# Kernel optimization log

Measured on AMD Instinct MI355X. Metric: run time of the kernel, lower is better.

## Reference

```python
import jax, jax.numpy as jnp
import numpy as np

B, T, D, H = 1024, 128, 300, 100
FORGET_BIAS = 1.0


def _lstm_final_c(x, W, b):
    """Run a BasicLSTMCell over x:[B,T,D]; return final cell state c:[B,H].
    Gate order (TF BasicLSTMCell): i, j, f, o from [x,h] @ W + b, W:[D+H,4H].
    """
    Bv = x.shape[0]
    c0 = jnp.zeros((Bv, H), x.dtype)
    h0 = jnp.zeros((Bv, H), x.dtype)

    def step(carry, xt):
        c, h = carry
        z = jnp.concatenate([xt, h], axis=-1) @ W + b  # [B,4H]
        i, j, f, o = jnp.split(z, 4, axis=-1)
        c2 = c * jax.nn.sigmoid(f + FORGET_BIAS) + jax.nn.sigmoid(i) * jnp.tanh(j)
        h2 = jnp.tanh(c2) * jax.nn.sigmoid(o)
        return (c2, h2), None

    (cT, _), _ = jax.lax.scan(step, (c0, h0), jnp.swapaxes(x, 0, 1))  # scan over time
    return cT


def _bi_rnn_c(x, W_fw, b_fw, W_bw, b_bw):
    # full sequence_length => backward cell consumes time-reversed input
    c_fw = _lstm_final_c(x, W_fw, b_fw)
    c_bw = _lstm_final_c(x[:, ::-1, :], W_bw, b_bw)
    return jnp.concatenate([c_fw, c_bw], axis=1)  # [B,2H]


def setup_inputs() -> dict:
    key = jax.random.key(0)
    ks = jax.random.split(key, 6)
    s = 0.05
    return {
        "premises": jax.random.normal(ks[0], (B, T, D), jnp.float32),
        "hypotheses": jax.random.normal(ks[1], (B, T, D), jnp.float32),
        "Wp_fw": jax.random.normal(ks[2], (D + H, 4 * H), jnp.float32) * s,
        "bp_fw": jnp.zeros((4 * H,), jnp.float32),
        "Wp_bw": jax.random.normal(ks[3], (D + H, 4 * H), jnp.float32) * s,
        "bp_bw": jnp.zeros((4 * H,), jnp.float32),
        "Wh_fw": jax.random.normal(ks[4], (D + H, 4 * H), jnp.float32) * s,
        "bh_fw": jnp.zeros((4 * H,), jnp.float32),
        "Wh_bw": jax.random.normal(ks[5], (D + H, 4 * H), jnp.float32) * s,
        "bh_bw": jnp.zeros((4 * H,), jnp.float32),
    }


def reference(premises, hypotheses, Wp_fw, bp_fw, Wp_bw, bp_bw,
              Wh_fw, bh_fw, Wh_bw, bh_bw):
    premise_out = _bi_rnn_c(premises, Wp_fw, bp_fw, Wp_bw, bp_bw)      # [B,2H]
    hypothesis_out = _bi_rnn_c(hypotheses, Wh_fw, bh_fw, Wh_bw, bh_bw)  # [B,2H]
    return jnp.concatenate([premise_out, hypothesis_out], axis=1)      # [B,4H]
```

## Files before the change

kernel.cpp:

```cpp
#include <hip/hip_runtime.h>
#include <hip/hip_bf16.h>

#define T_STEPS 128
#define D_IN    300
#define H_DIM   100
#define KDIM    400
#define KSTRIDE 424
#define NTILES  25
#define WAVES   12
#define BLOCK   (WAVES * 64)
#define MROWS   16
#define LN2E    1.44269504f
#define LN2E2   2.88539008f

typedef __attribute__((ext_vector_type(8))) short bf16x8;
typedef __attribute__((ext_vector_type(4))) float f32x4;

__device__ __forceinline__ ushort f2bf(float f) {
    uint u = __float_as_uint(f);
    u += 0x7FFFu + ((u >> 16) & 1u);
    return (ushort)(u >> 16);
}
__device__ __forceinline__ uint cvt_pk_bf16(float lo, float hi) {
    uint r;
    asm("v_cvt_pk_bf16_f32 %0, %1, %2" : "=v"(r) : "v"(lo), "v"(hi));
    return r;
}

__device__ __forceinline__ float lstm_gate(const f32x4 z, float& c) {
    float ei = __builtin_amdgcn_exp2f(-z[0]);
    float ej = __builtin_amdgcn_exp2f(fminf(-z[1], 126.0f));
    float ef = __builtin_amdgcn_exp2f(-z[2]);
    float eo = __builtin_amdgcn_exp2f(-z[3]);
    float rf  = __builtin_amdgcn_rcpf(1.0f + ef);
    float rij = __builtin_amdgcn_rcpf((1.0f + ei) * (1.0f + ej));
    float c2 = c * rf + (1.0f - ej) * rij;
    c = c2;
    float ec = __builtin_amdgcn_exp2f(fminf(-LN2E2 * c2, 126.0f));
    return (1.0f - ec) * __builtin_amdgcn_rcpf((1.0f + ec) * (1.0f + eo));
}

__global__ __launch_bounds__(256) void prep_w(
    const float* __restrict__ W0, const float* __restrict__ W1,
    const float* __restrict__ W2, const float* __restrict__ W3,
    ushort* __restrict__ Wt)
{
    int idx = blockIdx.x * 256 + threadIdx.x;
    const int total = 4 * 400 * KSTRIDE;
    if (idx >= total) return;
    int c   = idx / (400 * KSTRIDE);
    int rem = idx - c * (400 * KSTRIDE);
    int p   = rem / KSTRIDE;
    int k   = rem - p * KSTRIDE;
    const float* W = (c == 0) ? W0 : (c == 1) ? W1 : (c == 2) ? W2 : W3;
    const int g = p & 3;
    const float scale = (g == 1) ? LN2E2 : LN2E;
    float v = 0.0f;
    if (k < KDIM) v = W[k * 400 + g * 100 + (p >> 2)] * scale;
    Wt[idx] = f2bf(v);
}

__global__ __launch_bounds__(BLOCK) void lstm_mfma(
    const float* __restrict__ premises,
    const float* __restrict__ hypotheses,
    const float* __restrict__ b0, const float* __restrict__ b1,
    const float* __restrict__ b2, const float* __restrict__ b3,
    const ushort* __restrict__ Wt,
    float* __restrict__ out)
{
    __shared__ ushort xh[2][MROWS * KSTRIDE];
    __shared__ ushort b24[13 * 512];

    const int tid = threadIdx.x;
    const int l   = tid & 63;
    const int w   = tid >> 6;
    const int combo = blockIdx.y;
    const int row0  = blockIdx.x * MROWS;
    const bool backward = (combo & 1) != 0;
    const float* x    = (combo < 2) ? premises : hypotheses;
    const float* bias = (combo == 0) ? b0 : (combo == 1) ? b1 : (combo == 2) ? b2 : b3;
    const ushort* Wc  = Wt + (size_t)combo * 400 * KSTRIDE;

    const int bn = l & 15;
    const int ul = l >> 4;

    const int nt0 = 2 * w, nt1 = 2 * w + 1;
    bf16x8 bfr0[13], bfr1[13];
    {
        const ushort* bp = Wc + (size_t)(nt0 * 16 + bn) * KSTRIDE + ul * 8;
        #pragma unroll
        for (int ks = 0; ks < 13; ++ks)
            bfr0[ks] = *reinterpret_cast<const bf16x8*>(bp + ks * 32);
    }
    {
        const ushort* bp = Wc + (size_t)(nt1 * 16 + bn) * KSTRIDE + ul * 8;
        #pragma unroll
        for (int ks = 0; ks < 13; ++ks)
            bfr1[ks] = *reinterpret_cast<const bf16x8*>(bp + ks * 32);
    }
    const bool hasS = (w == WAVES - 1);

    if (w == 0) {
        const ushort* bp = Wc + (size_t)(24 * 16 + bn) * KSTRIDE + ul * 8;
        #pragma unroll
        for (int ks = 0; ks < 13; ++ks)
            *reinterpret_cast<bf16x8*>(&b24[ks * 512 + l * 8]) =
                *reinterpret_cast<const bf16x8*>(bp + ks * 32);
    }

    float bva[4], bvb[4], bvS[4] = {0.f, 0.f, 0.f, 0.f};
    {
        int u = nt0 * 4 + ul;
        bva[0] = LN2E * bias[u];
        bva[1] = LN2E2 * bias[100 + u];
        bva[2] = LN2E * (bias[200 + u] + 1.0f);
        bva[3] = LN2E * bias[300 + u];
        u = nt1 * 4 + ul;
        bvb[0] = LN2E * bias[u];
        bvb[1] = LN2E2 * bias[100 + u];
        bvb[2] = LN2E * (bias[200 + u] + 1.0f);
        bvb[3] = LN2E * bias[300 + u];
        if (hasS) {
            u = 96 + ul;
            bvS[0] = LN2E * bias[u];
            bvS[1] = LN2E2 * bias[100 + u];
            bvS[2] = LN2E * (bias[200 + u] + 1.0f);
            bvS[3] = LN2E * bias[300 + u];
        }
    }

    for (int i = tid; i < 2 * MROWS * (KSTRIDE - KDIM); i += BLOCK) {
        int b = i / (MROWS * (KSTRIDE - KDIM));
        int j = i - b * (MROWS * (KSTRIDE - KDIM));
        int r = j / (KSTRIDE - KDIM);
        int k = KDIM + (j - r * (KSTRIDE - KDIM));
        xh[b][r * KSTRIDE + k] = 0;
    }
    for (int i = tid; i < MROWS * H_DIM; i += BLOCK) {
        int r = i / H_DIM;
        xh[0][r * KSTRIDE + D_IN + (i - r * H_DIM)] = 0;
    }
    {
        int t0 = backward ? (T_STEPS - 1) : 0;
        for (int c = tid; c < 1200; c += BLOCK) {
            int r = c / 75, cc = c - (c / 75) * 75;
            float4 v = *reinterpret_cast<const float4*>(
                x + ((size_t)(row0 + r) * T_STEPS + t0) * D_IN + cc * 4);
            uint2 q;
            q.x = cvt_pk_bf16(v.x, v.y);
            q.y = cvt_pk_bf16(v.z, v.w);
            *reinterpret_cast<uint2*>(&xh[0][r * KSTRIDE + cc * 4]) = q;
        }
    }
    __syncthreads();

    const uint a_off = (uint)(l & 15) * KSTRIDE + (uint)(l >> 4) * 8;
    const int  row   = l & 15;
    const int sc0 = tid, sc1 = tid + BLOCK;
    const int sr0 = sc0 / 75, sd0 = sc0 - sr0 * 75;
    const int sr1 = sc1 / 75, sd1 = sc1 - sr1 * 75;
    const bool has1 = (sc1 < 1200);

    float creg0 = 0.f, creg1 = 0.f, cregS = 0.f;

    for (int t = 0; t < T_STEPS; ++t) {
        const ushort* cur = &xh[t & 1][0];
        ushort* nxt = &xh[(t & 1) ^ 1][0];

        float4 p0, p1;
        if (t < T_STEPS - 1) {
            int tn = backward ? (T_STEPS - 2 - t) : (t + 1);
            p0 = *reinterpret_cast<const float4*>(
                x + ((size_t)(row0 + sr0) * T_STEPS + tn) * D_IN + sd0 * 4);
            if (has1)
                p1 = *reinterpret_cast<const float4*>(
                    x + ((size_t)(row0 + sr1) * T_STEPS + tn) * D_IN + sd1 * 4);
        }

        f32x4 acc0 = {bva[0], bva[1], bva[2], bva[3]};
        f32x4 acc1 = {bvb[0], bvb[1], bvb[2], bvb[3]};
        f32x4 accS = {bvS[0], bvS[1], bvS[2], bvS[3]};
        #pragma unroll
        for (int ks = 0; ks < 13; ++ks) {
            const bf16x8 a = *reinterpret_cast<const bf16x8*>(cur + a_off + ks * 32);
            acc0 = __builtin_amdgcn_mfma_f32_16x16x32_bf16(bfr0[ks], a, acc0, 0, 0, 0);
            acc1 = __builtin_amdgcn_mfma_f32_16x16x32_bf16(bfr1[ks], a, acc1, 0, 0, 0);
            if (hasS) {
                const bf16x8 bs = *reinterpret_cast<const bf16x8*>(&b24[ks * 512 + l * 8]);
                accS = __builtin_amdgcn_mfma_f32_16x16x32_bf16(bs, a, accS, 0, 0, 0);
            }
        }

        float h0 = lstm_gate(acc0, creg0);
        float h1 = lstm_gate(acc1, creg1);
        uint pk = cvt_pk_bf16(h0, h1);
        nxt[row * KSTRIDE + D_IN + nt0 * 4 + ul] = (ushort)(pk & 0xFFFFu);
        nxt[row * KSTRIDE + D_IN + nt1 * 4 + ul] = (ushort)(pk >> 16);
        if (hasS) {
            float hS = lstm_gate(accS, cregS);
            nxt[row * KSTRIDE + D_IN + 96 + ul] = (ushort)(cvt_pk_bf16(hS, hS) & 0xFFFFu);
        }

        if (t < T_STEPS - 1) {
            uint2 q;
            q.x = cvt_pk_bf16(p0.x, p0.y);
            q.y = cvt_pk_bf16(p0.z, p0.w);
            *reinterpret_cast<uint2*>(&nxt[sr0 * KSTRIDE + sd0 * 4]) = q;
            if (has1) {
                q.x = cvt_pk_bf16(p1.x, p1.y);
                q.y = cvt_pk_bf16(p1.z, p1.w);
                *reinterpret_cast<uint2*>(&nxt[sr1 * KSTRIDE + sd1 * 4]) = q;
            }
        }
        __syncthreads();
    }

    out[(size_t)(row0 + row) * 400 + combo * 100 + nt0 * 4 + ul] = creg0;
    out[(size_t)(row0 + row) * 400 + combo * 100 + nt1 * 4 + ul] = creg1;
    if (hasS)
        out[(size_t)(row0 + row) * 400 + combo * 100 + 96 + ul] = cregS;
}

extern "C" void kernel_launch(void* const* d_in, const int* in_sizes, int n_in,
                              void* d_out, int out_size, void* d_ws, size_t ws_size,
                              hipStream_t stream) {
    const float* premises   = (const float*)d_in[0];
    const float* hypotheses = (const float*)d_in[1];
    const float* Wp_fw = (const float*)d_in[2];
    const float* bp_fw = (const float*)d_in[3];
    const float* Wp_bw = (const float*)d_in[4];
    const float* bp_bw = (const float*)d_in[5];
    const float* Wh_fw = (const float*)d_in[6];
    const float* bh_fw = (const float*)d_in[7];
    const float* Wh_bw = (const float*)d_in[8];
    const float* bh_bw = (const float*)d_in[9];
    float* out = (float*)d_out;
    ushort* Wt = (ushort*)d_ws;

    {
        const int total = 4 * 400 * KSTRIDE;
        prep_w<<<(total + 255) / 256, 256, 0, stream>>>(Wp_fw, Wp_bw, Wh_fw, Wh_bw, Wt);
    }
    dim3 grid(1024 / MROWS, 4);
    lstm_mfma<<<grid, dim3(BLOCK), 0, stream>>>(
        premises, hypotheses,
        bp_fw, bp_bw, bh_fw, bh_bw,
        Wt, out);
}
```

Measured before the change: 215.0 us.

## Use 8 waves with three N-tiles each and prefetch input two steps ahead

Measured after the change: 223.6 us. 1.04x slower.

```diff
diff --git a/kernel.cpp b/kernel.cpp
--- a/kernel.cpp
+++ b/kernel.cpp
@@ -6,10 +6,10 @@
 #define H_DIM   100
 #define KDIM    400
 #define KSTRIDE 424
-#define NTILES  25
-#define WAVES   12
+#define WAVES   8
 #define BLOCK   (WAVES * 64)
 #define MROWS   16
+#define NRES    3
 #define LN2E    1.44269504f
 #define LN2E2   2.88539008f
 
@@ -24,6 +24,11 @@
 __device__ __forceinline__ uint cvt_pk_bf16(float lo, float hi) {
     uint r;
     asm("v_cvt_pk_bf16_f32 %0, %1, %2" : "=v"(r) : "v"(lo), "v"(hi));
+    return r;
+}
+__device__ __forceinline__ bf16x8 gload16(const ushort* p) {
+    bf16x8 r;
+    asm volatile("global_load_dwordx4 %0, %1, off" : "=v"(r) : "v"(p));
     return r;
 }
 
@@ -60,7 +65,7 @@
     Wt[idx] = f2bf(v);
 }
 
-__global__ __launch_bounds__(BLOCK) void lstm_mfma(
+__global__ __launch_bounds__(BLOCK, 2) void lstm_mfma(
     const float* __restrict__ premises,
     const float* __restrict__ hypotheses,
     const float* __restrict__ b0, const float* __restrict__ b1,
@@ -84,22 +89,17 @@
     const int bn = l & 15;
     const int ul = l >> 4;
 
-    const int nt0 = 2 * w, nt1 = 2 * w + 1;
-    bf16x8 bfr0[13], bfr1[13];
-    {
-        const ushort* bp = Wc + (size_t)(nt0 * 16 + bn) * KSTRIDE + ul * 8;
+    bf16x8 bfr[NRES][13];
+    #pragma unroll
+    for (int i = 0; i < NRES; ++i) {
+        const ushort* bp = Wc + (size_t)((3 * w + i) * 16 + bn) * KSTRIDE + ul * 8;
         #pragma unroll
         for (int ks = 0; ks < 13; ++ks)
-            bfr0[ks] = *reinterpret_cast<const bf16x8*>(bp + ks * 32);
-    }
-    {
-        const ushort* bp = Wc + (size_t)(nt1 * 16 + bn) * KSTRIDE + ul * 8;
-        #pragma unroll
-        for (int ks = 0; ks < 13; ++ks)
-            bfr1[ks] = *reinterpret_cast<const bf16x8*>(bp + ks * 32);
-    }
+            bfr[i][ks] = gload16(bp + ks * 32);
+    }
+    asm volatile("s_waitcnt vmcnt(0)" ::: "memory");
+
     const bool hasS = (w == WAVES - 1);
-
     if (w == 0) {
         const ushort* bp = Wc + (size_t)(24 * 16 + bn) * KSTRIDE + ul * 8;
         #pragma unroll
@@ -108,25 +108,21 @@
                 *reinterpret_cast<const bf16x8*>(bp + ks * 32);
     }
 
-    float bva[4], bvb[4], bvS[4] = {0.f, 0.f, 0.f, 0.f};
-    {
-        int u = nt0 * 4 + ul;
-        bva[0] = LN2E * bias[u];
-        bva[1] = LN2E2 * bias[100 + u];
-        bva[2] = LN2E * (bias[200 + u] + 1.0f);
-        bva[3] = LN2E * bias[300 + u];
-        u = nt1 * 4 + ul;
-        bvb[0] = LN2E * bias[u];
-        bvb[1] = LN2E2 * bias[100 + u];
-        bvb[2] = LN2E * (bias[200 + u] + 1.0f);
-        bvb[3] = LN2E * bias[300 + u];
-        if (hasS) {
-            u = 96 + ul;
-            bvS[0] = LN2E * bias[u];
-            bvS[1] = LN2E2 * bias[100 + u];
-            bvS[2] = LN2E * (bias[200 + u] + 1.0f);
-            bvS[3] = LN2E * bias[300 + u];
-        }
+    float bv[NRES][4], bvS[4] = {0.f, 0.f, 0.f, 0.f};
+    #pragma unroll
+    for (int i = 0; i < NRES; ++i) {
+        int u = (3 * w + i) * 4 + ul;
+        bv[i][0] = LN2E * bias[u];
+        bv[i][1] = LN2E2 * bias[100 + u];
+        bv[i][2] = LN2E * (bias[200 + u] + 1.0f);
+        bv[i][3] = LN2E * bias[300 + u];
+    }
+    if (hasS) {
+        int u = 96 + ul;
+        bvS[0] = LN2E * bias[u];
+        bvS[1] = LN2E2 * bias[100 + u];
+        bvS[2] = LN2E * (bias[200 + u] + 1.0f);
+        bvS[3] = LN2E * bias[300 + u];
     }
 
     for (int i = tid; i < 2 * MROWS * (KSTRIDE - KDIM); i += BLOCK) {
@@ -156,35 +152,54 @@
 
     const uint a_off = (uint)(l & 15) * KSTRIDE + (uint)(l >> 4) * 8;
     const int  row   = l & 15;
-    const int sc0 = tid, sc1 = tid + BLOCK;
+    const bool stager = (tid < 448);
+    const int sc0 = tid, sc1 = tid + 448, sc2 = tid + 896;
     const int sr0 = sc0 / 75, sd0 = sc0 - sr0 * 75;
     const int sr1 = sc1 / 75, sd1 = sc1 - sr1 * 75;
-    const bool has1 = (sc1 < 1200);
-
-    float creg0 = 0.f, creg1 = 0.f, cregS = 0.f;
-
-    for (int t = 0; t < T_STEPS; ++t) {
+    const int sr2 = sc2 / 75, sd2 = sc2 - sr2 * 75;
+    const bool has2 = (sc2 < 1200);
+
+    float creg0 = 0.f, creg1 = 0.f, creg2 = 0.f, cregS = 0.f;
+
+    float4 A0, A1, A2, B0, B1, B2;
+
+    if (stager) {
+        int tn = backward ? (T_STEPS - 2) : 1;
+        A0 = *reinterpret_cast<const float4*>(
+            x + ((size_t)(row0 + sr0) * T_STEPS + tn) * D_IN + sd0 * 4);
+        A1 = *reinterpret_cast<const float4*>(
+            x + ((size_t)(row0 + sr1) * T_STEPS + tn) * D_IN + sd1 * 4);
+        if (has2)
+            A2 = *reinterpret_cast<const float4*>(
+                x + ((size_t)(row0 + sr2) * T_STEPS + tn) * D_IN + sd2 * 4);
+    }
+
+    auto step = [&](int t, float4& i0, float4& i1, float4& i2,
+                           float4& u0, float4& u1, float4& u2) {
         const ushort* cur = &xh[t & 1][0];
         ushort* nxt = &xh[(t & 1) ^ 1][0];
 
-        float4 p0, p1;
-        if (t < T_STEPS - 1) {
-            int tn = backward ? (T_STEPS - 2 - t) : (t + 1);
-            p0 = *reinterpret_cast<const float4*>(
+        if (t < T_STEPS - 2 && stager) {
+            int tn = backward ? (T_STEPS - 3 - t) : (t + 2);
+            i0 = *reinterpret_cast<const float4*>(
                 x + ((size_t)(row0 + sr0) * T_STEPS + tn) * D_IN + sd0 * 4);
-            if (has1)
-                p1 = *reinterpret_cast<const float4*>(
-                    x + ((size_t)(row0 + sr1) * T_STEPS + tn) * D_IN + sd1 * 4);
-        }
-
-        f32x4 acc0 = {bva[0], bva[1], bva[2], bva[3]};
-        f32x4 acc1 = {bvb[0], bvb[1], bvb[2], bvb[3]};
+            i1 = *reinterpret_cast<const float4*>(
+                x + ((size_t)(row0 + sr1) * T_STEPS + tn) * D_IN + sd1 * 4);
+            if (has2)
+                i2 = *reinterpret_cast<const float4*>(
+                    x + ((size_t)(row0 + sr2) * T_STEPS + tn) * D_IN + sd2 * 4);
+        }
+
+        f32x4 acc0 = {bv[0][0], bv[0][1], bv[0][2], bv[0][3]};
+        f32x4 acc1 = {bv[1][0], bv[1][1], bv[1][2], bv[1][3]};
+        f32x4 acc2 = {bv[2][0], bv[2][1], bv[2][2], bv[2][3]};
         f32x4 accS = {bvS[0], bvS[1], bvS[2], bvS[3]};
         #pragma unroll
         for (int ks = 0; ks < 13; ++ks) {
             const bf16x8 a = *reinterpret_cast<const bf16x8*>(cur + a_off + ks * 32);
-            acc0 = __builtin_amdgcn_mfma_f32_16x16x32_bf16(bfr0[ks], a, acc0, 0, 0, 0);
-            acc1 = __builtin_amdgcn_mfma_f32_16x16x32_bf16(bfr1[ks], a, acc1, 0, 0, 0);
+            acc0 = __builtin_amdgcn_mfma_f32_16x16x32_bf16(bfr[0][ks], a, acc0, 0, 0, 0);
+            acc1 = __builtin_amdgcn_mfma_f32_16x16x32_bf16(bfr[1][ks], a, acc1, 0, 0, 0);
+            acc2 = __builtin_amdgcn_mfma_f32_16x16x32_bf16(bfr[2][ks], a, acc2, 0, 0, 0);
             if (hasS) {
                 const bf16x8 bs = *reinterpret_cast<const bf16x8*>(&b24[ks * 512 + l * 8]);
                 accS = __builtin_amdgcn_mfma_f32_16x16x32_bf16(bs, a, accS, 0, 0, 0);
@@ -193,30 +208,43 @@
 
         float h0 = lstm_gate(acc0, creg0);
         float h1 = lstm_gate(acc1, creg1);
-        uint pk = cvt_pk_bf16(h0, h1);
-        nxt[row * KSTRIDE + D_IN + nt0 * 4 + ul] = (ushort)(pk & 0xFFFFu);
-        nxt[row * KSTRIDE + D_IN + nt1 * 4 + ul] = (ushort)(pk >> 16);
+        float h2 = lstm_gate(acc2, creg2);
+        uint pk01 = cvt_pk_bf16(h0, h1);
+        uint pk2  = cvt_pk_bf16(h2, h2);
+        ushort* hdst = nxt + row * KSTRIDE + D_IN + (3 * w) * 4 + ul;
+        hdst[0] = (ushort)(pk01 & 0xFFFFu);
+        hdst[4] = (ushort)(pk01 >> 16);
+        hdst[8] = (ushort)(pk2 & 0xFFFFu);
         if (hasS) {
             float hS = lstm_gate(accS, cregS);
             nxt[row * KSTRIDE + D_IN + 96 + ul] = (ushort)(cvt_pk_bf16(hS, hS) & 0xFFFFu);
         }
 
-        if (t < T_STEPS - 1) {
+        if (t < T_STEPS - 1 && stager) {
             uint2 q;
-            q.x = cvt_pk_bf16(p0.x, p0.y);
-            q.y = cvt_pk_bf16(p0.z, p0.w);
+            q.x = cvt_pk_bf16(u0.x, u0.y);
+            q.y = cvt_pk_bf16(u0.z, u0.w);
             *reinterpret_cast<uint2*>(&nxt[sr0 * KSTRIDE + sd0 * 4]) = q;
-            if (has1) {
-                q.x = cvt_pk_bf16(p1.x, p1.y);
-                q.y = cvt_pk_bf16(p1.z, p1.w);
-                *reinterpret_cast<uint2*>(&nxt[sr1 * KSTRIDE + sd1 * 4]) = q;
+            q.x = cvt_pk_bf16(u1.x, u1.y);
+            q.y = cvt_pk_bf16(u1.z, u1.w);
+            *reinterpret_cast<uint2*>(&nxt[sr1 * KSTRIDE + sd1 * 4]) = q;
+            if (has2) {
+                q.x = cvt_pk_bf16(u2.x, u2.y);
+                q.y = cvt_pk_bf16(u2.z, u2.w);
+                *reinterpret_cast<uint2*>(&nxt[sr2 * KSTRIDE + sd2 * 4]) = q;
             }
         }
         __syncthreads();
-    }
-
-    out[(size_t)(row0 + row) * 400 + combo * 100 + nt0 * 4 + ul] = creg0;
-    out[(size_t)(row0 + row) * 400 + combo * 100 + nt1 * 4 + ul] = creg1;
+    };
+
+    for (int t = 0; t < T_STEPS; t += 2) {
+        step(t,     B0, B1, B2, A0, A1, A2);
+        step(t + 1, A0, A1, A2, B0, B1, B2);
+    }
+
+    out[(size_t)(row0 + row) * 400 + combo * 100 + (3 * w) * 4 + ul]     = creg0;
+    out[(size_t)(row0 + row) * 400 + combo * 100 + (3 * w + 1) * 4 + ul] = creg1;
+    out[(size_t)(row0 + row) * 400 + combo * 100 + (3 * w + 2) * 4 + ul] = creg2;
     if (hasS)
         out[(size_t)(row0 + row) * 400 + combo * 100 + 96 + ul] = cregS;
 }
```
